# Performance work log

Measured on AMD Instinct MI355X. Metric: run time of the kernel, lower is better.

## Reference

```python
import jax, jax.numpy as jnp
import numpy as np

# SLAYER neuron params (from network.yaml defaults)
THETA = 10.0      # spike threshold
TAU_SR = 10.0     # synaptic (PSP) time constant
TAU_REF = 1.0     # refractory time constant
SCALE_REF = 2.0   # refractory strength (in units of theta)
TAU_RHO = 1.0     # surrogate-gradient width
SCALE_RHO = 1.0   # surrogate-gradient scale
TS = 1.0          # simulation timestep


@jax.custom_vjp
def spike_heaviside(u):
    # SLAYER spike generation: hard threshold in forward
    return (u >= THETA).astype(u.dtype)

def _spk_fwd(u):
    return spike_heaviside(u), u

def _spk_bwd(u, g):
    # SLAYER surrogate: rho(u) = (scaleRho/tauRho) * exp(-|u - theta| / tauRho)
    surr = (SCALE_RHO / TAU_RHO) * jnp.exp(-jnp.abs(u - THETA) / TAU_RHO)
    return (g * surr,)

spike_heaviside.defvjp(_spk_fwd, _spk_bwd)


def psp(x):
    """Temporal post-synaptic-potential filter (exponential synapse kernel).
    x: (B, T, F) -> (B, T, F);  p[t] = decay * p[t-1] + x[t]."""
    decay = jnp.exp(jnp.asarray(-TS / TAU_SR, x.dtype))
    def step(p, xt):
        p = decay * p + xt
        return p, p
    p0 = jnp.zeros((x.shape[0], x.shape[2]), x.dtype)
    _, ps = jax.lax.scan(step, p0, jnp.swapaxes(x, 0, 1))  # scan over T
    return jnp.swapaxes(ps, 0, 1)


def spike(u):
    """Thresholded spike generation with refractory feedback.
    u: (B, T, F) membrane input; refractory state subtracts 2*theta after a spike
    and decays with tauRef (SLAYER refractory response)."""
    decay_ref = jnp.exp(jnp.asarray(-TS / TAU_REF, u.dtype))
    def step(r, ut):
        v = ut + r
        s = spike_heaviside(v)
        r = decay_ref * (r - SCALE_REF * THETA * s)
        return r, s
    r0 = jnp.zeros((u.shape[0], u.shape[2]), u.dtype)
    _, ss = jax.lax.scan(step, r0, jnp.swapaxes(u, 0, 1))  # scan over T
    return jnp.swapaxes(ss, 0, 1)


def setup_inputs() -> dict:
    key = jax.random.key(0)
    k1, k2, k3 = jax.random.split(key, 3)
    B, T, F_IN, F_H, F_OUT = 64, 500, 1250, 512, 2
    x = (jax.random.uniform(k1, (B, T, F_IN)) < 0.1).astype(jnp.float32)
    W1 = jax.random.normal(k2, (F_H, F_IN), jnp.float32) * 0.05
    W2 = jax.random.normal(k3, (F_OUT, F_H), jnp.float32) * 0.05
    return {"x": x, "W1": W1, "W2": W2}


def reference(x, W1, W2):
    # layer 1: dense projection per timestep -> PSP filter -> spike
    s1 = spike(psp(jnp.einsum('btf,hf->bth', x, W1)))   # (B, T, 512)
    # layer 2
    out = spike(psp(jnp.einsum('bth,oh->bto', s1, W2))) # (B, T, 2)
    return out
```

## Files before the change

kernel.cpp:

```cpp
#include <hip/hip_runtime.h>
#include <hip/hip_bf16.h>
#include <cstdint>
#include <cstddef>

#define B_N   64
#define T_N   500
#define K_IN  1250
#define KP    1280
#define N_H   512
#define M_N   32000

#define BM 128
#define BN 128
#define BK 32
#define NT (KP / BK)

typedef __attribute__((ext_vector_type(8))) short bf16x8;
typedef __attribute__((ext_vector_type(4))) float f32x4;

#define DECAY_SR  0.9048374180359595732f
#define DECAY_REF 0.3678794411714423216f
#define THETA 10.0f

__device__ __forceinline__ unsigned short f2bf(float f) {
  __hip_bfloat16 h = __float2bfloat16(f);
  return *reinterpret_cast<unsigned short*>(&h);
}
__device__ __forceinline__ uint32_t f2bf2(float a, float b) {
  float2 t; t.x = a; t.y = b;
  __hip_bfloat162 h = __float22bfloat162_rn(t);
  return *reinterpret_cast<uint32_t*>(&h);
}
__device__ __forceinline__ float bf2f(unsigned short s) {
  union { uint32_t u; float f; } v; v.u = ((uint32_t)s) << 16; return v.f;
}

__global__ __launch_bounds__(256) void w1cvt_kernel(const float* __restrict__ W1,
                                                    short* __restrict__ W1b) {
  int k = blockIdx.x * 256 + threadIdx.x;
  int n = blockIdx.y;
  float v = (k < K_IN) ? W1[(size_t)n * K_IN + k] : 0.f;
  W1b[(size_t)n * KP + k] = (short)f2bf(v);
}

__global__ __launch_bounds__(256) void gemm1_kernel(const float* __restrict__ X,
                                                    const short* __restrict__ W1b,
                                                    unsigned short* __restrict__ U1) {
  __shared__ short As[2][BM * BK];
  __shared__ short Bs[2][BN * BK];
  const int tid  = threadIdx.x;
  const int bm   = blockIdx.x * BM;
  const int bn   = blockIdx.y * BN;
  const int w    = tid >> 6;
  const int lane = tid & 63;
  const int wr   = w >> 1;
  const int wc   = w & 1;
  const int lrow = lane & 15;
  const int lgrp = lane >> 4;

  f32x4 acc[4][4];
  #pragma unroll
  for (int i = 0; i < 4; ++i)
    #pragma unroll
    for (int j = 0; j < 4; ++j)
      acc[i][j] = (f32x4){0.f, 0.f, 0.f, 0.f};

  const int arow  = tid >> 2;
  const int aslot = tid & 3;
  const int bch0  = w * 2;
  const int brow  = lane >> 2;
  const int bslp  = lane & 3;

  auto stage = [&](int buf, int k0) {
    #pragma unroll
    for (int c = 0; c < 2; ++c) {
      int ch = bch0 + c;
      int n  = ch * 16 + brow;
      int ss = bslp ^ ((n >> 1) & 3);
      const short* src = W1b + (size_t)(bn + n) * KP + k0 + ss * 8;
      __builtin_amdgcn_global_load_lds(
          (const __attribute__((address_space(1))) void*)src,
          (__attribute__((address_space(3))) void*)&Bs[buf][ch * 512], 16, 0, 0);
    }
    #pragma unroll
    for (int rr = 0; rr < 2; ++rr) {
      int row = arow + rr * 64;
      int gk  = k0 + aslot * 8;
      const float* s = X + (size_t)(bm + row) * K_IN + gk;
      float v0, v1, v2, v3, v4, v5, v6, v7;
      if (gk + 7 < K_IN) {
        float2 x0 = *(const float2*)(s);
        float2 x1 = *(const float2*)(s + 2);
        float2 x2 = *(const float2*)(s + 4);
        float2 x3 = *(const float2*)(s + 6);
        v0 = x0.x; v1 = x0.y; v2 = x1.x; v3 = x1.y;
        v4 = x2.x; v5 = x2.y; v6 = x3.x; v7 = x3.y;
      } else {
        v0 = (gk + 0 < K_IN) ? s[0] : 0.f;
        v1 = (gk + 1 < K_IN) ? s[1] : 0.f;
        v2 = (gk + 2 < K_IN) ? s[2] : 0.f;
        v3 = (gk + 3 < K_IN) ? s[3] : 0.f;
        v4 = (gk + 4 < K_IN) ? s[4] : 0.f;
        v5 = (gk + 5 < K_IN) ? s[5] : 0.f;
        v6 = (gk + 6 < K_IN) ? s[6] : 0.f;
        v7 = (gk + 7 < K_IN) ? s[7] : 0.f;
      }
      uint4 pk;
      pk.x = f2bf2(v0, v1); pk.y = f2bf2(v2, v3);
      pk.z = f2bf2(v4, v5); pk.w = f2bf2(v6, v7);
      *(uint4*)&As[buf][row * BK + ((aslot ^ ((row >> 1) & 3)) * 8)] = pk;
    }
  };

  stage(0, 0);
  __syncthreads();
  int pb = 0;
  for (int t = 0; t < NT; ++t) {
    if (t + 1 < NT) stage(pb ^ 1, (t + 1) * BK);
    bf16x8 af[4], bv[4];
    #pragma unroll
    for (int i = 0; i < 4; ++i) {
      int r = wr * 64 + i * 16 + lrow;
      af[i] = *(const bf16x8*)&As[pb][r * BK + ((lgrp ^ ((r >> 1) & 3)) * 8)];
    }
    #pragma unroll
    for (int j = 0; j < 4; ++j) {
      int r = wc * 64 + j * 16 + lrow;
      bv[j] = *(const bf16x8*)&Bs[pb][r * BK + ((lgrp ^ ((r >> 1) & 3)) * 8)];
    }
    #pragma unroll
    for (int i = 0; i < 4; ++i)
      #pragma unroll
      for (int j = 0; j < 4; ++j)
        acc[i][j] = __builtin_amdgcn_mfma_f32_16x16x32_bf16(af[i], bv[j], acc[i][j], 0, 0, 0);
    __syncthreads();
    pb ^= 1;
  }

  #pragma unroll
  for (int i = 0; i < 4; ++i) {
    int row0 = bm + wr * 64 + i * 16 + lgrp * 4;
    #pragma unroll
    for (int j = 0; j < 4; ++j) {
      int col = bn + wc * 64 + j * 16 + lrow;
      #pragma unroll
      for (int r = 0; r < 4; ++r)
        U1[(size_t)(row0 + r) * N_H + col] = f2bf(acc[i][j][r]);
    }
  }
}

__global__ __launch_bounds__(128) void scan1_kernel(const unsigned short* __restrict__ U1,
                                                    unsigned long long* __restrict__ S1m) {
  int idx  = blockIdx.x * 128 + threadIdx.x;
  int b    = idx >> 9, h = idx & 511;
  int lane = threadIdx.x & 63;
  const unsigned short* u = U1 + (size_t)b * T_N * N_H + h;
  unsigned long long* mout = S1m + (size_t)b * T_N * 8 + (h >> 6);
  float p = 0.f, r = 0.f;
  float bufA[10], bufB[10];

  auto load = [&](float* buf, int t0) {
    #pragma unroll
    for (int j = 0; j < 10; ++j) buf[j] = bf2f(u[(size_t)(t0 + j) * N_H]);
  };
  auto proc = [&](const float* buf, int t0) {
    #pragma unroll
    for (int j = 0; j < 10; ++j) {
      p = DECAY_SR * p + buf[j];
      float v = p + r;
      bool sp = (v >= THETA);
      r = DECAY_REF * (r - (sp ? 2.f * THETA : 0.f));
      unsigned long long bal = __ballot(sp);
      if (lane == 0) mout[(size_t)(t0 + j) * 8] = bal;
    }
  };

  load(bufA, 0);
  for (int g = 0; g < 25; ++g) {
    int ta = g * 20, tb = ta + 10;
    load(bufB, tb);
    proc(bufA, ta);
    if (g < 24) load(bufA, tb + 10);
    proc(bufB, tb);
  }
}

__global__ __launch_bounds__(256) void gemm2_kernel(const unsigned char* __restrict__ S1b,
                                                    const float* __restrict__ W2,
                                                    float* __restrict__ U2) {
  int m    = blockIdx.x * 4 + (threadIdx.x >> 6);
  int lane = threadIdx.x & 63;
  unsigned int byte = S1b[(size_t)m * 64 + lane];
  float a0 = 0.f, a1 = 0.f;
  #pragma unroll
  for (int j = 0; j < 8; ++j) {
    int h = lane * 8 + j;
    float sel = ((byte >> j) & 1u) ? 1.f : 0.f;
    a0 += sel * W2[h];
    a1 += sel * W2[N_H + h];
  }
  #pragma unroll
  for (int off = 32; off >= 1; off >>= 1) {
    a0 += __shfl_down(a0, off);
    a1 += __shfl_down(a1, off);
  }
  if (lane == 0) {
    U2[(size_t)m * 2]     = a0;
    U2[(size_t)m * 2 + 1] = a1;
  }
}

__global__ __launch_bounds__(128) void scan2_kernel(const float* __restrict__ U2,
                                                    float* __restrict__ OUT) {
  __shared__ float lu[T_N * 2];
  __shared__ float ls[T_N * 2];
  int b = blockIdx.x;
  const float* src = U2 + (size_t)b * T_N * 2;
  for (int i = threadIdx.x; i < T_N * 2; i += 128) lu[i] = src[i];
  __syncthreads();
  if (threadIdx.x < 2) {
    int o = threadIdx.x;
    float p = 0.f, r = 0.f;
    for (int t = 0; t < T_N; ++t) {
      p = DECAY_SR * p + lu[t * 2 + o];
      float v = p + r;
      float sp = (v >= THETA) ? 1.f : 0.f;
      r = DECAY_REF * (r - 2.f * THETA * sp);
      ls[t * 2 + o] = sp;
    }
  }
  __syncthreads();
  float* dst = OUT + (size_t)b * T_N * 2;
  for (int i = threadIdx.x; i < T_N * 2; i += 128) dst[i] = ls[i];
}

extern "C" void kernel_launch(void* const* d_in, const int* in_sizes, int n_in,
                              void* d_out, int out_size, void* d_ws, size_t ws_size,
                              hipStream_t stream) {
  const float* X  = (const float*)d_in[0];
  const float* W1 = (const float*)d_in[1];
  const float* W2 = (const float*)d_in[2];
  float* OUT = (float*)d_out;

  char* ws = (char*)d_ws;
  short*              W1b = (short*)ws;
  unsigned short*     U1  = (unsigned short*)(ws + 1310720);
  unsigned long long* S1m = (unsigned long long*)(ws + 34078720);
  float*              U2  = (float*)(ws + 36126720);

  w1cvt_kernel<<<dim3(KP / 256, N_H), 256, 0, stream>>>(W1, W1b);
  gemm1_kernel<<<dim3(M_N / BM, N_H / BN), 256, 0, stream>>>(X, W1b, U1);
  scan1_kernel<<<dim3((B_N * N_H) / 128), 128, 0, stream>>>(U1, S1m);
  gemm2_kernel<<<dim3(M_N / 4), 256, 0, stream>>>((const unsigned char*)S1m, W2, U2);
  scan2_kernel<<<dim3(B_N), 128, 0, stream>>>(U2, OUT);
}
```

Baseline: 387.9 us.

## Retile GEMM1 so each block covers full hidden width, reading X once

```diff
diff --git a/kernel.cpp b/kernel.cpp
--- a/kernel.cpp
+++ b/kernel.cpp
@@ -10,8 +10,7 @@
 #define N_H   512
 #define M_N   32000
 
-#define BM 128
-#define BN 128
+#define BM 64
 #define BK 32
 #define NT (KP / BK)
 
@@ -47,46 +46,42 @@
                                                     const short* __restrict__ W1b,
                                                     unsigned short* __restrict__ U1) {
   __shared__ short As[2][BM * BK];
-  __shared__ short Bs[2][BN * BK];
+  __shared__ short Bs[2][N_H * BK];
   const int tid  = threadIdx.x;
   const int bm   = blockIdx.x * BM;
-  const int bn   = blockIdx.y * BN;
   const int w    = tid >> 6;
   const int lane = tid & 63;
-  const int wr   = w >> 1;
-  const int wc   = w & 1;
   const int lrow = lane & 15;
   const int lgrp = lane >> 4;
-
-  f32x4 acc[4][4];
+  const int lsw  = lgrp ^ ((lrow >> 1) & 3);
+
+  f32x4 acc[4][8];
   #pragma unroll
   for (int i = 0; i < 4; ++i)
     #pragma unroll
-    for (int j = 0; j < 4; ++j)
+    for (int j = 0; j < 8; ++j)
       acc[i][j] = (f32x4){0.f, 0.f, 0.f, 0.f};
 
   const int arow  = tid >> 2;
   const int aslot = tid & 3;
-  const int bch0  = w * 2;
-  const int brow  = lane >> 2;
-  const int bslp  = lane & 3;
+  const int awofs = arow * BK + ((aslot ^ ((arow >> 1) & 3)) * 8);
+  const int brow16 = lane >> 2;
+  const int bslp   = lane & 3;
 
   auto stage = [&](int buf, int k0) {
     #pragma unroll
-    for (int c = 0; c < 2; ++c) {
-      int ch = bch0 + c;
-      int n  = ch * 16 + brow;
+    for (int c = 0; c < 8; ++c) {
+      int n  = w * 128 + c * 16 + brow16;
       int ss = bslp ^ ((n >> 1) & 3);
-      const short* src = W1b + (size_t)(bn + n) * KP + k0 + ss * 8;
+      const short* src = W1b + (size_t)n * KP + k0 + ss * 8;
       __builtin_amdgcn_global_load_lds(
           (const __attribute__((address_space(1))) void*)src,
-          (__attribute__((address_space(3))) void*)&Bs[buf][ch * 512], 16, 0, 0);
-    }
-    #pragma unroll
-    for (int rr = 0; rr < 2; ++rr) {
-      int row = arow + rr * 64;
-      int gk  = k0 + aslot * 8;
-      const float* s = X + (size_t)(bm + row) * K_IN + gk;
+          (__attribute__((address_space(3))) void*)&Bs[buf][(w * 128 + c * 16) * BK],
+          16, 0, 0);
+    }
+    {
+      int gk = k0 + aslot * 8;
+      const float* s = X + (size_t)(bm + arow) * K_IN + gk;
       float v0, v1, v2, v3, v4, v5, v6, v7;
       if (gk + 7 < K_IN) {
         float2 x0 = *(const float2*)(s);
@@ -108,7 +103,7 @@
       uint4 pk;
       pk.x = f2bf2(v0, v1); pk.y = f2bf2(v2, v3);
       pk.z = f2bf2(v4, v5); pk.w = f2bf2(v6, v7);
-      *(uint4*)&As[buf][row * BK + ((aslot ^ ((row >> 1) & 3)) * 8)] = pk;
+      *(uint4*)&As[buf][awofs] = pk;
     }
   };
 
@@ -117,21 +112,17 @@
   int pb = 0;
   for (int t = 0; t < NT; ++t) {
     if (t + 1 < NT) stage(pb ^ 1, (t + 1) * BK);
-    bf16x8 af[4], bv[4];
-    #pragma unroll
-    for (int i = 0; i < 4; ++i) {
-      int r = wr * 64 + i * 16 + lrow;
-      af[i] = *(const bf16x8*)&As[pb][r * BK + ((lgrp ^ ((r >> 1) & 3)) * 8)];
-    }
-    #pragma unroll
-    for (int j = 0; j < 4; ++j) {
-      int r = wc * 64 + j * 16 + lrow;
-      bv[j] = *(const bf16x8*)&Bs[pb][r * BK + ((lgrp ^ ((r >> 1) & 3)) * 8)];
-    }
+    bf16x8 af[4], bv[8];
+    #pragma unroll
+    for (int i = 0; i < 4; ++i)
+      af[i] = *(const bf16x8*)&As[pb][(i * 16 + lrow) * BK + lsw * 8];
+    #pragma unroll
+    for (int j = 0; j < 8; ++j)
+      bv[j] = *(const bf16x8*)&Bs[pb][(w * 128 + j * 16 + lrow) * BK + lsw * 8];
     #pragma unroll
     for (int i = 0; i < 4; ++i)
       #pragma unroll
-      for (int j = 0; j < 4; ++j)
+      for (int j = 0; j < 8; ++j)
         acc[i][j] = __builtin_amdgcn_mfma_f32_16x16x32_bf16(af[i], bv[j], acc[i][j], 0, 0, 0);
     __syncthreads();
     pb ^= 1;
@@ -139,10 +130,10 @@
 
   #pragma unroll
   for (int i = 0; i < 4; ++i) {
-    int row0 = bm + wr * 64 + i * 16 + lgrp * 4;
-    #pragma unroll
-    for (int j = 0; j < 4; ++j) {
-      int col = bn + wc * 64 + j * 16 + lrow;
+    int row0 = bm + i * 16 + lgrp * 4;
+    #pragma unroll
+    for (int j = 0; j < 8; ++j) {
+      int col = w * 128 + j * 16 + lrow;
       #pragma unroll
       for (int r = 0; r < 4; ++r)
         U1[(size_t)(row0 + r) * N_H + col] = f2bf(acc[i][j][r]);
@@ -250,7 +241,7 @@
   float*              U2  = (float*)(ws + 36126720);
 
   w1cvt_kernel<<<dim3(KP / 256, N_H), 256, 0, stream>>>(W1, W1b);
-  gemm1_kernel<<<dim3(M_N / BM, N_H / BN), 256, 0, stream>>>(X, W1b, U1);
+  gemm1_kernel<<<dim3(M_N / BM), 256, 0, stream>>>(X, W1b, U1);
   scan1_kernel<<<dim3((B_N * N_H) / 128), 128, 0, stream>>>(U1, S1m);
   gemm2_kernel<<<dim3(M_N / 4), 256, 0, stream>>>((const unsigned char*)S1m, W2, U2);
   scan2_kernel<<<dim3(B_N), 128, 0, stream>>>(U2, OUT);
```

After: 382.0 us. No clear change (-1.5%).
